# Kernel tuning notes

Measured on AMD Instinct MI355X. Metric: run time of the kernel, lower is better.

Reference implementation:

```python
import jax, jax.numpy as jnp
import numpy as np

B, D, H, STEPS = 32768, 8, 64, 100


def setup_inputs() -> dict:
    key = jax.random.key(0)
    ks = jax.random.split(key, 7)
    def lin(k, shape, fan_in):
        # torch nn.Linear default init: U(-1/sqrt(fan_in), 1/sqrt(fan_in))
        return jax.random.uniform(k, shape, jnp.float32, -1.0, 1.0) / np.sqrt(fan_in).astype(np.float32)
    return {
        "x0": jax.random.normal(ks[0], (B, D), jnp.float32),
        "W1": lin(ks[1], (H, D + 1), D + 1),
        "b1": lin(ks[2], (H,), D + 1),
        "W2": lin(ks[3], (H, H), H),
        "b2": lin(ks[4], (H,), H),
        "W3": lin(ks[5], (D, H), H),
        "b3": lin(ks[6], (D,), H),
        "num_steps": STEPS,
    }


def _mlp(x, t_col, W1, b1, W2, b2, W3, b3):
    # x: [B, D], t_col: [B, 1] -> dx/dt: [B, D]
    xt = jnp.concatenate([x, t_col], axis=1)          # [B, D+1]
    h = jnp.tanh(xt @ W1.T + b1)                      # [B, H]
    h = jnp.tanh(h @ W2.T + b2)                       # [B, H]
    return h @ W3.T + b3                              # [B, D]


def reference(x0, W1, b1, W2, b2, W3, b3, num_steps):
    t0, t1 = 0.0, 1.0
    dt = (t1 - t0) / num_steps
    n, d = x0.shape
    ones_out = jnp.ones((n, d), x0.dtype)

    def step(carry, i):
        x, ld = carry
        t_col = jnp.full((n, 1), t0, x0.dtype) + i.astype(x0.dtype) * dt
        dx = _mlp(x, t_col, W1, b1, W2, b2, W3, b3)
        x_new = x + dt * dx
        # Faithful to torch source: grad of dx_dt.sum() wrt x evaluated at the
        # POST-step x (this is J^T @ 1, then summed over input dims).
        f = lambda xx: _mlp(xx, t_col, W1, b1, W2, b2, W3, b3)
        _, vjp_fn = jax.vjp(f, x_new)
        (g,) = vjp_fn(ones_out)                       # [B, D]
        ld_new = ld + dt * g.sum(axis=1)
        return (x_new, ld_new), None

    init = (x0, jnp.zeros(n, x0.dtype))
    (x, log_det), _ = jax.lax.scan(step, init, jnp.arange(num_steps))
    return x, log_det
```

## Files before the change

### kernel.cpp

```cpp
#include <hip/hip_runtime.h>


__device__ float g_w1r[64];
__device__ float g_w3c[64];

__global__ void cnf_prep(const float* __restrict__ W1, const float* __restrict__ W3) {
    int h = threadIdx.x;
    float s = 0.f;
#pragma unroll
    for (int k = 0; k < 8; ++k) s += W1[h * 9 + k];
    g_w1r[h] = s;
    float c = 0.f;
#pragma unroll
    for (int d = 0; d < 8; ++d) c += W3[d * 64 + h];
    g_w3c[h] = c;
}

__device__ __forceinline__ float ftanh(float x) {
    float e = __builtin_amdgcn_exp2f(x * 2.885390081777926815f);
    float r = __builtin_amdgcn_rcpf(e + 1.0f);
    return fmaf(-2.0f, r, 1.0f);
}

typedef __attribute__((ext_vector_type(8))) short v8s;
typedef __attribute__((ext_vector_type(4))) float v4f;
typedef __attribute__((ext_vector_type(2))) float v2f;

union FragU {
    v8s s;
    unsigned u[4];
};

__device__ __forceinline__ unsigned pkbf(float a, float b) {
    unsigned ua = __builtin_bit_cast(unsigned, a) + 0x8000u;
    unsigned ub = __builtin_bit_cast(unsigned, b) + 0x8000u;
    return __builtin_amdgcn_perm(ub, ua, 0x07060302u);
}
__device__ __forceinline__ unsigned pkbf2(v2f v) { return pkbf(v.x, v.y); }

__device__ __forceinline__ int physj(int ks, int q, int jj) {
    return 16 * (ks + 2 * (jj >> 2)) + 4 * q + (jj & 3);
}

__device__ __forceinline__ void rename(const uint2 ph[4], FragU bh[2]) {
#pragma unroll
    for (int ks = 0; ks < 2; ++ks) {
        bh[ks].u[0] = ph[ks].x;
        bh[ks].u[1] = ph[ks].y;
        bh[ks].u[2] = ph[ks + 2].x;
        bh[ks].u[3] = ph[ks + 2].y;
    }
}

__global__ __launch_bounds__(256, 2) void cnf_fused(
    const float* __restrict__ x0, const float* __restrict__ W1,
    const float* __restrict__ b1, const float* __restrict__ W2,
    const float* __restrict__ b2, const float* __restrict__ W3,
    const float* __restrict__ b3, const int* __restrict__ nsp,
    float* __restrict__ out, int rows) {
    const int tid = threadIdx.x;
    const int w = tid >> 6;
    const int lane = tid & 63;
    const int c = lane & 15;
    const int q = lane >> 4;
    const int row0 = blockIdx.x * 64 + w * 16;

    const int n = *nsp;
    const float dt = 1.0f / (float)n;

    FragU a1[4];
#pragma unroll
    for (int mt = 0; mt < 4; ++mt) {
        const int m = 16 * mt + c;
        float f[8] = {0.f, 0.f, 0.f, 0.f, 0.f, 0.f, 0.f, 0.f};
        if (q == 0) {
#pragma unroll
            for (int jj = 0; jj < 4; ++jj) f[jj] = W1[m * 9 + jj];
            f[4] = W1[m * 9 + 8];
            f[5] = b1[m];
        } else if (q == 1) {
#pragma unroll
            for (int jj = 0; jj < 4; ++jj) f[jj] = W1[m * 9 + 4 + jj];
        }
#pragma unroll
        for (int p = 0; p < 4; ++p) a1[mt].u[p] = pkbf(f[2 * p], f[2 * p + 1]);
    }
    FragU a2[4][2], a2u[4][2], a2d[4][2];
#pragma unroll
    for (int mt = 0; mt < 4; ++mt)
#pragma unroll
        for (int ks = 0; ks < 2; ++ks) {
            const int m = 16 * mt + c;
            float f[8], fu[8], fd[8];
#pragma unroll
            for (int jj = 0; jj < 8; ++jj) {
                const int pj = physj(ks, q, jj);
                const float wv = W2[m * 64 + pj];
                f[jj] = wv;
                fu[jj] = wv * g_w1r[pj];
                fd[jj] = wv * (dt * W1[pj * 9 + 8]);
            }
#pragma unroll
            for (int p = 0; p < 4; ++p) {
                a2[mt][ks].u[p] = pkbf(f[2 * p], f[2 * p + 1]);
                a2u[mt][ks].u[p] = pkbf(fu[2 * p], fu[2 * p + 1]);
                a2d[mt][ks].u[p] = pkbf(fd[2 * p], fd[2 * p + 1]);
            }
        }
    FragU a3[2];
#pragma unroll
    for (int ks = 0; ks < 2; ++ks) {
        float f[8];
#pragma unroll
        for (int jj = 0; jj < 8; ++jj) f[jj] = W3[(c & 7) * 64 + physj(ks, q, jj)];
#pragma unroll
        for (int p = 0; p < 4; ++p) a3[ks].u[p] = pkbf(f[2 * p], f[2 * p + 1]);
    }
    v2f w3c01[4], w3c23[4];
    v4f vb2[4];
#pragma unroll
    for (int mt = 0; mt < 4; ++mt) {
        const int j0 = 16 * mt + 4 * q;
        vb2[mt][0] = b2[j0]; vb2[mt][1] = b2[j0 + 1];
        vb2[mt][2] = b2[j0 + 2]; vb2[mt][3] = b2[j0 + 3];
        w3c01[mt] = v2f{g_w3c[j0], g_w3c[j0 + 1]};
        w3c23[mt] = v2f{g_w3c[j0 + 2], g_w3c[j0 + 3]};
    }
    v4f vb3;
#pragma unroll
    for (int r = 0; r < 4; ++r) vb3[r] = b3[(4 * q + r) & 7];

    float xr[4];
    {
        float4 v = *(const float4*)(x0 + (size_t)(row0 + c) * 8 + 4 * (q & 1));
        xr[0] = v.x; xr[1] = v.y; xr[2] = v.z; xr[3] = v.w;
    }
    const v4f vzero = {0.f, 0.f, 0.f, 0.f};
    v2f gv = {0.f, 0.f};

    {
        FragU bx;
        bx.u[0] = pkbf(xr[0], xr[1]);
        bx.u[1] = pkbf(xr[2], xr[3]);
        bx.u[2] = pkbf(0.0f, 1.0f);
        bx.u[3] = 0u;
        v4f d1[4];
#pragma unroll
        for (int mt = 0; mt < 4; ++mt)
            d1[mt] = __builtin_amdgcn_mfma_f32_16x16x32_bf16(a1[mt].s, bx.s, vzero, 0, 0, 0);
        uint2 ph[4];
#pragma unroll
        for (int mt = 0; mt < 4; ++mt) {
            ph[mt].x = pkbf(ftanh(d1[mt][0]), ftanh(d1[mt][1]));
            ph[mt].y = pkbf(ftanh(d1[mt][2]), ftanh(d1[mt][3]));
        }
        FragU bh[2];
        rename(ph, bh);
        v4f d2[4];
#pragma unroll
        for (int mt = 0; mt < 4; ++mt) {
            d2[mt] = __builtin_amdgcn_mfma_f32_16x16x32_bf16(a2[mt][0].s, bh[0].s, vb2[mt], 0, 0, 0);
            d2[mt] = __builtin_amdgcn_mfma_f32_16x16x32_bf16(a2[mt][1].s, bh[1].s, d2[mt], 0, 0, 0);
        }
#pragma unroll
        for (int mt = 0; mt < 4; ++mt) {
            ph[mt].x = pkbf(ftanh(d2[mt][0]), ftanh(d2[mt][1]));
            ph[mt].y = pkbf(ftanh(d2[mt][2]), ftanh(d2[mt][3]));
        }
        FragU bh2[2];
        rename(ph, bh2);
        v4f d3;
        d3 = __builtin_amdgcn_mfma_f32_16x16x32_bf16(a3[0].s, bh2[0].s, vb3, 0, 0, 0);
        d3 = __builtin_amdgcn_mfma_f32_16x16x32_bf16(a3[1].s, bh2[1].s, d3, 0, 0, 0);
#pragma unroll
        for (int r = 0; r < 4; ++r) xr[r] = fmaf(dt, d3[r], xr[r]);
    }

    float tp = 0.0f;
    for (int i = 1; i < n; ++i) {
        FragU bx;
        bx.u[0] = pkbf(xr[0], xr[1]);
        bx.u[1] = pkbf(xr[2], xr[3]);
        bx.u[2] = pkbf(tp, 1.0f);
        bx.u[3] = 0u;
        tp += dt;
        v4f d1[4];
#pragma unroll
        for (int mt = 0; mt < 4; ++mt)
            d1[mt] = __builtin_amdgcn_mfma_f32_16x16x32_bf16(a1[mt].s, bx.s, vzero, 0, 0, 0);

        uint2 phb[4], pom[4];
#pragma unroll
        for (int mt = 0; mt < 4; ++mt) {
            v2f th01 = {ftanh(d1[mt][0]), ftanh(d1[mt][1])};
            v2f th23 = {ftanh(d1[mt][2]), ftanh(d1[mt][3])};
            v2f om01 = v2f{1.f, 1.f} - th01 * th01;
            v2f om23 = v2f{1.f, 1.f} - th23 * th23;
            phb[mt].x = pkbf2(th01);
            phb[mt].y = pkbf2(th23);
            pom[mt].x = pkbf2(om01);
            pom[mt].y = pkbf2(om23);
        }
        FragU bhb[2], bo[2];
        rename(phb, bhb);
        rename(pom, bo);

        v4f z2b[4], sv[4], dz2[4];
#pragma unroll
        for (int mt = 0; mt < 4; ++mt) {
            z2b[mt] = __builtin_amdgcn_mfma_f32_16x16x32_bf16(a2[mt][0].s, bhb[0].s, vb2[mt], 0, 0, 0);
            z2b[mt] = __builtin_amdgcn_mfma_f32_16x16x32_bf16(a2[mt][1].s, bhb[1].s, z2b[mt], 0, 0, 0);
            sv[mt] = __builtin_amdgcn_mfma_f32_16x16x32_bf16(a2u[mt][0].s, bo[0].s, vzero, 0, 0, 0);
            sv[mt] = __builtin_amdgcn_mfma_f32_16x16x32_bf16(a2u[mt][1].s, bo[1].s, sv[mt], 0, 0, 0);
            dz2[mt] = __builtin_amdgcn_mfma_f32_16x16x32_bf16(a2d[mt][0].s, bo[0].s, vzero, 0, 0, 0);
            dz2[mt] = __builtin_amdgcn_mfma_f32_16x16x32_bf16(a2d[mt][1].s, bo[1].s, dz2[mt], 0, 0, 0);
        }

        uint2 ph2[4];
#pragma unroll
        for (int mt = 0; mt < 4; ++mt) {
            v2f th01 = {ftanh(z2b[mt][0]), ftanh(z2b[mt][1])};
            v2f th23 = {ftanh(z2b[mt][2]), ftanh(z2b[mt][3])};
            v2f om01 = v2f{1.f, 1.f} - th01 * th01;
            v2f om23 = v2f{1.f, 1.f} - th23 * th23;
            gv += (w3c01[mt] * om01) * v2f{sv[mt][0], sv[mt][1]};
            gv += (w3c23[mt] * om23) * v2f{sv[mt][2], sv[mt][3]};
            v2f tf01 = om01 * v2f{dz2[mt][0], dz2[mt][1]} + th01;
            v2f tf23 = om23 * v2f{dz2[mt][2], dz2[mt][3]} + th23;
            ph2[mt].x = pkbf2(tf01);
            ph2[mt].y = pkbf2(tf23);
        }
        FragU bh2[2];
        rename(ph2, bh2);
        v4f d3;
        d3 = __builtin_amdgcn_mfma_f32_16x16x32_bf16(a3[0].s, bh2[0].s, vb3, 0, 0, 0);
        d3 = __builtin_amdgcn_mfma_f32_16x16x32_bf16(a3[1].s, bh2[1].s, d3, 0, 0, 0);
#pragma unroll
        for (int r = 0; r < 4; ++r) xr[r] = fmaf(dt, d3[r], xr[r]);
    }

    {
        FragU bx;
        bx.u[0] = pkbf(xr[0], xr[1]);
        bx.u[1] = pkbf(xr[2], xr[3]);
        bx.u[2] = pkbf(tp, 1.0f);
        bx.u[3] = 0u;
        v4f d1[4];
#pragma unroll
        for (int mt = 0; mt < 4; ++mt)
            d1[mt] = __builtin_amdgcn_mfma_f32_16x16x32_bf16(a1[mt].s, bx.s, vzero, 0, 0, 0);
        uint2 phb[4], pom[4];
#pragma unroll
        for (int mt = 0; mt < 4; ++mt) {
            v2f th01 = {ftanh(d1[mt][0]), ftanh(d1[mt][1])};
            v2f th23 = {ftanh(d1[mt][2]), ftanh(d1[mt][3])};
            v2f om01 = v2f{1.f, 1.f} - th01 * th01;
            v2f om23 = v2f{1.f, 1.f} - th23 * th23;
            phb[mt].x = pkbf2(th01);
            phb[mt].y = pkbf2(th23);
            pom[mt].x = pkbf2(om01);
            pom[mt].y = pkbf2(om23);
        }
        FragU bhb[2], bo[2];
        rename(phb, bhb);
        rename(pom, bo);
        v4f z2b[4], sv[4];
#pragma unroll
        for (int mt = 0; mt < 4; ++mt) {
            z2b[mt] = __builtin_amdgcn_mfma_f32_16x16x32_bf16(a2[mt][0].s, bhb[0].s, vb2[mt], 0, 0, 0);
            z2b[mt] = __builtin_amdgcn_mfma_f32_16x16x32_bf16(a2[mt][1].s, bhb[1].s, z2b[mt], 0, 0, 0);
            sv[mt] = __builtin_amdgcn_mfma_f32_16x16x32_bf16(a2u[mt][0].s, bo[0].s, vzero, 0, 0, 0);
            sv[mt] = __builtin_amdgcn_mfma_f32_16x16x32_bf16(a2u[mt][1].s, bo[1].s, sv[mt], 0, 0, 0);
        }
#pragma unroll
        for (int mt = 0; mt < 4; ++mt) {
            v2f th01 = {ftanh(z2b[mt][0]), ftanh(z2b[mt][1])};
            v2f th23 = {ftanh(z2b[mt][2]), ftanh(z2b[mt][3])};
            v2f om01 = v2f{1.f, 1.f} - th01 * th01;
            v2f om23 = v2f{1.f, 1.f} - th23 * th23;
            gv += (w3c01[mt] * om01) * v2f{sv[mt][0], sv[mt][1]};
            gv += (w3c23[mt] * om23) * v2f{sv[mt][2], sv[mt][3]};
        }
    }

    float g = gv.x + gv.y;
    g += __shfl_xor(g, 16);
    g += __shfl_xor(g, 32);
    if (q < 2) {
        float4 st = {xr[0], xr[1], xr[2], xr[3]};
        *(float4*)(out + (size_t)(row0 + c) * 8 + 4 * q) = st;
    }
    if (q == 0) out[(size_t)rows * 8 + row0 + c] = dt * g;
}

extern "C" void kernel_launch(void* const* d_in, const int* in_sizes, int n_in,
                              void* d_out, int out_size, void* d_ws, size_t ws_size,
                              hipStream_t stream) {
    const float* x0 = (const float*)d_in[0];
    const float* W1 = (const float*)d_in[1];
    const float* b1 = (const float*)d_in[2];
    const float* W2 = (const float*)d_in[3];
    const float* b2 = (const float*)d_in[4];
    const float* W3 = (const float*)d_in[5];
    const float* b3 = (const float*)d_in[6];
    const int* ns = (const int*)d_in[7];
    float* out = (float*)d_out;
    const int rows = in_sizes[0] / 8;

    hipLaunchKernelGGL(cnf_prep, dim3(1), dim3(64), 0, stream, W1, W3);
    hipLaunchKernelGGL(cnf_fused, dim3(rows / 64), dim3(256), 0, stream,
                       x0, W1, b1, W2, b2, W3, b3, ns, out, rows);
}
```

Measured before the change: 226.7 us.

## Switch MFMA operands to fp16 and fold tanh scale and w3c into weights

Replaces bf16 packing (add-and-perm) with the hardware cvt_pkrtz fp16 pack and swaps to f16 MFMA. Pre-multiplies W1, b1, W2 and b2 by the exp2 tanh scale so ftanh drops a multiply per element. Folds the w3c column sums into the a2u weight matrix so the gradient accumulation loses one multiply and eight registers. This trims VALU work in the step loop, at the cost of fp16 range and rounding risk from the scaled weights and round-toward-zero conversion.

```diff
diff --git a/kernel.cpp b/kernel.cpp
--- a/kernel.cpp
+++ b/kernel.cpp
@@ -1,5 +1,7 @@
 #include <hip/hip_runtime.h>
 
+
+#define TSCALE 2.885390081777926815f
 
 __device__ float g_w1r[64];
 __device__ float g_w3c[64];
@@ -16,27 +18,27 @@
     g_w3c[h] = c;
 }
 
-__device__ __forceinline__ float ftanh(float x) {
-    float e = __builtin_amdgcn_exp2f(x * 2.885390081777926815f);
+__device__ __forceinline__ float ftanh_s(float z) {
+    float e = __builtin_amdgcn_exp2f(z);
     float r = __builtin_amdgcn_rcpf(e + 1.0f);
     return fmaf(-2.0f, r, 1.0f);
 }
 
-typedef __attribute__((ext_vector_type(8))) short v8s;
+typedef __attribute__((ext_vector_type(8))) _Float16 v8h;
+typedef __attribute__((ext_vector_type(2))) __fp16 v2fp;
 typedef __attribute__((ext_vector_type(4))) float v4f;
 typedef __attribute__((ext_vector_type(2))) float v2f;
 
 union FragU {
-    v8s s;
+    v8h h;
     unsigned u[4];
 };
 
-__device__ __forceinline__ unsigned pkbf(float a, float b) {
-    unsigned ua = __builtin_bit_cast(unsigned, a) + 0x8000u;
-    unsigned ub = __builtin_bit_cast(unsigned, b) + 0x8000u;
-    return __builtin_amdgcn_perm(ub, ua, 0x07060302u);
-}
-__device__ __forceinline__ unsigned pkbf2(v2f v) { return pkbf(v.x, v.y); }
+__device__ __forceinline__ unsigned pk16(float a, float b) {
+    v2fp t = __builtin_amdgcn_cvt_pkrtz(a, b);
+    return __builtin_bit_cast(unsigned, t);
+}
+__device__ __forceinline__ unsigned pk16v(v2f v) { return pk16(v.x, v.y); }
 
 __device__ __forceinline__ int physj(int ks, int q, int jj) {
     return 16 * (ks + 2 * (jj >> 2)) + 4 * q + (jj & 3);
@@ -75,36 +77,37 @@
         float f[8] = {0.f, 0.f, 0.f, 0.f, 0.f, 0.f, 0.f, 0.f};
         if (q == 0) {
 #pragma unroll
-            for (int jj = 0; jj < 4; ++jj) f[jj] = W1[m * 9 + jj];
-            f[4] = W1[m * 9 + 8];
-            f[5] = b1[m];
+            for (int jj = 0; jj < 4; ++jj) f[jj] = TSCALE * W1[m * 9 + jj];
+            f[4] = TSCALE * W1[m * 9 + 8];
+            f[5] = TSCALE * b1[m];
         } else if (q == 1) {
 #pragma unroll
-            for (int jj = 0; jj < 4; ++jj) f[jj] = W1[m * 9 + 4 + jj];
-        }
-#pragma unroll
-        for (int p = 0; p < 4; ++p) a1[mt].u[p] = pkbf(f[2 * p], f[2 * p + 1]);
-    }
-    FragU a2[4][2], a2u[4][2], a2d[4][2];
+            for (int jj = 0; jj < 4; ++jj) f[jj] = TSCALE * W1[m * 9 + 4 + jj];
+        }
+#pragma unroll
+        for (int p = 0; p < 4; ++p) a1[mt].u[p] = pk16(f[2 * p], f[2 * p + 1]);
+    }
+    FragU a2[4][2], a2g[4][2], a2d[4][2];
 #pragma unroll
     for (int mt = 0; mt < 4; ++mt)
 #pragma unroll
         for (int ks = 0; ks < 2; ++ks) {
             const int m = 16 * mt + c;
-            float f[8], fu[8], fd[8];
+            const float w3cm = g_w3c[m];
+            float f[8], fg[8], fd[8];
 #pragma unroll
             for (int jj = 0; jj < 8; ++jj) {
                 const int pj = physj(ks, q, jj);
                 const float wv = W2[m * 64 + pj];
-                f[jj] = wv;
-                fu[jj] = wv * g_w1r[pj];
+                f[jj] = TSCALE * wv;
+                fg[jj] = w3cm * wv * g_w1r[pj];
                 fd[jj] = wv * (dt * W1[pj * 9 + 8]);
             }
 #pragma unroll
             for (int p = 0; p < 4; ++p) {
-                a2[mt][ks].u[p] = pkbf(f[2 * p], f[2 * p + 1]);
-                a2u[mt][ks].u[p] = pkbf(fu[2 * p], fu[2 * p + 1]);
-                a2d[mt][ks].u[p] = pkbf(fd[2 * p], fd[2 * p + 1]);
+                a2[mt][ks].u[p] = pk16(f[2 * p], f[2 * p + 1]);
+                a2g[mt][ks].u[p] = pk16(fg[2 * p], fg[2 * p + 1]);
+                a2d[mt][ks].u[p] = pk16(fd[2 * p], fd[2 * p + 1]);
             }
         }
     FragU a3[2];
@@ -114,17 +117,14 @@
 #pragma unroll
         for (int jj = 0; jj < 8; ++jj) f[jj] = W3[(c & 7) * 64 + physj(ks, q, jj)];
 #pragma unroll
-        for (int p = 0; p < 4; ++p) a3[ks].u[p] = pkbf(f[2 * p], f[2 * p + 1]);
-    }
-    v2f w3c01[4], w3c23[4];
+        for (int p = 0; p < 4; ++p) a3[ks].u[p] = pk16(f[2 * p], f[2 * p + 1]);
+    }
     v4f vb2[4];
 #pragma unroll
     for (int mt = 0; mt < 4; ++mt) {
         const int j0 = 16 * mt + 4 * q;
-        vb2[mt][0] = b2[j0]; vb2[mt][1] = b2[j0 + 1];
-        vb2[mt][2] = b2[j0 + 2]; vb2[mt][3] = b2[j0 + 3];
-        w3c01[mt] = v2f{g_w3c[j0], g_w3c[j0 + 1]};
-        w3c23[mt] = v2f{g_w3c[j0 + 2], g_w3c[j0 + 3]};
+        vb2[mt][0] = TSCALE * b2[j0]; vb2[mt][1] = TSCALE * b2[j0 + 1];
+        vb2[mt][2] = TSCALE * b2[j0 + 2]; vb2[mt][3] = TSCALE * b2[j0 + 3];
     }
     v4f vb3;
 #pragma unroll
@@ -140,38 +140,38 @@
 
     {
         FragU bx;
-        bx.u[0] = pkbf(xr[0], xr[1]);
-        bx.u[1] = pkbf(xr[2], xr[3]);
-        bx.u[2] = pkbf(0.0f, 1.0f);
+        bx.u[0] = pk16(xr[0], xr[1]);
+        bx.u[1] = pk16(xr[2], xr[3]);
+        bx.u[2] = pk16(0.0f, 1.0f);
         bx.u[3] = 0u;
         v4f d1[4];
 #pragma unroll
         for (int mt = 0; mt < 4; ++mt)
-            d1[mt] = __builtin_amdgcn_mfma_f32_16x16x32_bf16(a1[mt].s, bx.s, vzero, 0, 0, 0);
+            d1[mt] = __builtin_amdgcn_mfma_f32_16x16x32_f16(a1[mt].h, bx.h, vzero, 0, 0, 0);
         uint2 ph[4];
 #pragma unroll
         for (int mt = 0; mt < 4; ++mt) {
-            ph[mt].x = pkbf(ftanh(d1[mt][0]), ftanh(d1[mt][1]));
-            ph[mt].y = pkbf(ftanh(d1[mt][2]), ftanh(d1[mt][3]));
+            ph[mt].x = pk16(ftanh_s(d1[mt][0]), ftanh_s(d1[mt][1]));
+            ph[mt].y = pk16(ftanh_s(d1[mt][2]), ftanh_s(d1[mt][3]));
         }
         FragU bh[2];
         rename(ph, bh);
         v4f d2[4];
 #pragma unroll
         for (int mt = 0; mt < 4; ++mt) {
-            d2[mt] = __builtin_amdgcn_mfma_f32_16x16x32_bf16(a2[mt][0].s, bh[0].s, vb2[mt], 0, 0, 0);
-            d2[mt] = __builtin_amdgcn_mfma_f32_16x16x32_bf16(a2[mt][1].s, bh[1].s, d2[mt], 0, 0, 0);
-        }
-#pragma unroll
-        for (int mt = 0; mt < 4; ++mt) {
-            ph[mt].x = pkbf(ftanh(d2[mt][0]), ftanh(d2[mt][1]));
-            ph[mt].y = pkbf(ftanh(d2[mt][2]), ftanh(d2[mt][3]));
+            d2[mt] = __builtin_amdgcn_mfma_f32_16x16x32_f16(a2[mt][0].h, bh[0].h, vb2[mt], 0, 0, 0);
+            d2[mt] = __builtin_amdgcn_mfma_f32_16x16x32_f16(a2[mt][1].h, bh[1].h, d2[mt], 0, 0, 0);
+        }
+#pragma unroll
+        for (int mt = 0; mt < 4; ++mt) {
+            ph[mt].x = pk16(ftanh_s(d2[mt][0]), ftanh_s(d2[mt][1]));
+            ph[mt].y = pk16(ftanh_s(d2[mt][2]), ftanh_s(d2[mt][3]));
         }
         FragU bh2[2];
         rename(ph, bh2);
         v4f d3;
-        d3 = __builtin_amdgcn_mfma_f32_16x16x32_bf16(a3[0].s, bh2[0].s, vb3, 0, 0, 0);
-        d3 = __builtin_amdgcn_mfma_f32_16x16x32_bf16(a3[1].s, bh2[1].s, d3, 0, 0, 0);
+        d3 = __builtin_amdgcn_mfma_f32_16x16x32_f16(a3[0].h, bh2[0].h, vb3, 0, 0, 0);
+        d3 = __builtin_amdgcn_mfma_f32_16x16x32_f16(a3[1].h, bh2[1].h, d3, 0, 0, 0);
 #pragma unroll
         for (int r = 0; r < 4; ++r) xr[r] = fmaf(dt, d3[r], xr[r]);
     }
@@ -179,107 +179,107 @@
     float tp = 0.0f;
     for (int i = 1; i < n; ++i) {
         FragU bx;
-        bx.u[0] = pkbf(xr[0], xr[1]);
-        bx.u[1] = pkbf(xr[2], xr[3]);
-        bx.u[2] = pkbf(tp, 1.0f);
+        bx.u[0] = pk16(xr[0], xr[1]);
+        bx.u[1] = pk16(xr[2], xr[3]);
+        bx.u[2] = pk16(tp, 1.0f);
         bx.u[3] = 0u;
         tp += dt;
         v4f d1[4];
 #pragma unroll
         for (int mt = 0; mt < 4; ++mt)
-            d1[mt] = __builtin_amdgcn_mfma_f32_16x16x32_bf16(a1[mt].s, bx.s, vzero, 0, 0, 0);
+            d1[mt] = __builtin_amdgcn_mfma_f32_16x16x32_f16(a1[mt].h, bx.h, vzero, 0, 0, 0);
 
         uint2 phb[4], pom[4];
 #pragma unroll
         for (int mt = 0; mt < 4; ++mt) {
-            v2f th01 = {ftanh(d1[mt][0]), ftanh(d1[mt][1])};
-            v2f th23 = {ftanh(d1[mt][2]), ftanh(d1[mt][3])};
+            v2f th01 = {ftanh_s(d1[mt][0]), ftanh_s(d1[mt][1])};
+            v2f th23 = {ftanh_s(d1[mt][2]), ftanh_s(d1[mt][3])};
             v2f om01 = v2f{1.f, 1.f} - th01 * th01;
             v2f om23 = v2f{1.f, 1.f} - th23 * th23;
-            phb[mt].x = pkbf2(th01);
-            phb[mt].y = pkbf2(th23);
-            pom[mt].x = pkbf2(om01);
-            pom[mt].y = pkbf2(om23);
+            phb[mt].x = pk16v(th01);
+            phb[mt].y = pk16v(th23);
+            pom[mt].x = pk16v(om01);
+            pom[mt].y = pk16v(om23);
         }
         FragU bhb[2], bo[2];
         rename(phb, bhb);
         rename(pom, bo);
 
-        v4f z2b[4], sv[4], dz2[4];
-#pragma unroll
-        for (int mt = 0; mt < 4; ++mt) {
-            z2b[mt] = __builtin_amdgcn_mfma_f32_16x16x32_bf16(a2[mt][0].s, bhb[0].s, vb2[mt], 0, 0, 0);
-            z2b[mt] = __builtin_amdgcn_mfma_f32_16x16x32_bf16(a2[mt][1].s, bhb[1].s, z2b[mt], 0, 0, 0);
-            sv[mt] = __builtin_amdgcn_mfma_f32_16x16x32_bf16(a2u[mt][0].s, bo[0].s, vzero, 0, 0, 0);
-            sv[mt] = __builtin_amdgcn_mfma_f32_16x16x32_bf16(a2u[mt][1].s, bo[1].s, sv[mt], 0, 0, 0);
-            dz2[mt] = __builtin_amdgcn_mfma_f32_16x16x32_bf16(a2d[mt][0].s, bo[0].s, vzero, 0, 0, 0);
-            dz2[mt] = __builtin_amdgcn_mfma_f32_16x16x32_bf16(a2d[mt][1].s, bo[1].s, dz2[mt], 0, 0, 0);
+        v4f z2b[4], sg[4], dz2[4];
+#pragma unroll
+        for (int mt = 0; mt < 4; ++mt) {
+            z2b[mt] = __builtin_amdgcn_mfma_f32_16x16x32_f16(a2[mt][0].h, bhb[0].h, vb2[mt], 0, 0, 0);
+            z2b[mt] = __builtin_amdgcn_mfma_f32_16x16x32_f16(a2[mt][1].h, bhb[1].h, z2b[mt], 0, 0, 0);
+            sg[mt] = __builtin_amdgcn_mfma_f32_16x16x32_f16(a2g[mt][0].h, bo[0].h, vzero, 0, 0, 0);
+            sg[mt] = __builtin_amdgcn_mfma_f32_16x16x32_f16(a2g[mt][1].h, bo[1].h, sg[mt], 0, 0, 0);
+            dz2[mt] = __builtin_amdgcn_mfma_f32_16x16x32_f16(a2d[mt][0].h, bo[0].h, vzero, 0, 0, 0);
+            dz2[mt] = __builtin_amdgcn_mfma_f32_16x16x32_f16(a2d[mt][1].h, bo[1].h, dz2[mt], 0, 0, 0);
         }
 
         uint2 ph2[4];
 #pragma unroll
         for (int mt = 0; mt < 4; ++mt) {
-            v2f th01 = {ftanh(z2b[mt][0]), ftanh(z2b[mt][1])};
-            v2f th23 = {ftanh(z2b[mt][2]), ftanh(z2b[mt][3])};
+            v2f th01 = {ftanh_s(z2b[mt][0]), ftanh_s(z2b[mt][1])};
+            v2f th23 = {ftanh_s(z2b[mt][2]), ftanh_s(z2b[mt][3])};
             v2f om01 = v2f{1.f, 1.f} - th01 * th01;
             v2f om23 = v2f{1.f, 1.f} - th23 * th23;
-            gv += (w3c01[mt] * om01) * v2f{sv[mt][0], sv[mt][1]};
-            gv += (w3c23[mt] * om23) * v2f{sv[mt][2], sv[mt][3]};
+            gv += om01 * v2f{sg[mt][0], sg[mt][1]};
+            gv += om23 * v2f{sg[mt][2], sg[mt][3]};
             v2f tf01 = om01 * v2f{dz2[mt][0], dz2[mt][1]} + th01;
             v2f tf23 = om23 * v2f{dz2[mt][2], dz2[mt][3]} + th23;
-            ph2[mt].x = pkbf2(tf01);
-            ph2[mt].y = pkbf2(tf23);
+            ph2[mt].x = pk16v(tf01);
+            ph2[mt].y = pk16v(tf23);
         }
         FragU bh2[2];
         rename(ph2, bh2);
         v4f d3;
-        d3 = __builtin_amdgcn_mfma_f32_16x16x32_bf16(a3[0].s, bh2[0].s, vb3, 0, 0, 0);
-        d3 = __builtin_amdgcn_mfma_f32_16x16x32_bf16(a3[1].s, bh2[1].s, d3, 0, 0, 0);
+        d3 = __builtin_amdgcn_mfma_f32_16x16x32_f16(a3[0].h, bh2[0].h, vb3, 0, 0, 0);
+        d3 = __builtin_amdgcn_mfma_f32_16x16x32_f16(a3[1].h, bh2[1].h, d3, 0, 0, 0);
 #pragma unroll
         for (int r = 0; r < 4; ++r) xr[r] = fmaf(dt, d3[r], xr[r]);
     }
 
     {
         FragU bx;
-        bx.u[0] = pkbf(xr[0], xr[1]);
-        bx.u[1] = pkbf(xr[2], xr[3]);
-        bx.u[2] = pkbf(tp, 1.0f);
+        bx.u[0] = pk16(xr[0], xr[1]);
+        bx.u[1] = pk16(xr[2], xr[3]);
+        bx.u[2] = pk16(tp, 1.0f);
         bx.u[3] = 0u;
         v4f d1[4];
 #pragma unroll
         for (int mt = 0; mt < 4; ++mt)
-            d1[mt] = __builtin_amdgcn_mfma_f32_16x16x32_bf16(a1[mt].s, bx.s, vzero, 0, 0, 0);
+            d1[mt] = __builtin_amdgcn_mfma_f32_16x16x32_f16(a1[mt].h, bx.h, vzero, 0, 0, 0);
         uint2 phb[4], pom[4];
 #pragma unroll
         for (int mt = 0; mt < 4; ++mt) {
-            v2f th01 = {ftanh(d1[mt][0]), ftanh(d1[mt][1])};
-            v2f th23 = {ftanh(d1[mt][2]), ftanh(d1[mt][3])};
+            v2f th01 = {ftanh_s(d1[mt][0]), ftanh_s(d1[mt][1])};
+            v2f th23 = {ftanh_s(d1[mt][2]), ftanh_s(d1[mt][3])};
             v2f om01 = v2f{1.f, 1.f} - th01 * th01;
             v2f om23 = v2f{1.f, 1.f} - th23 * th23;
-            phb[mt].x = pkbf2(th01);
-            phb[mt].y = pkbf2(th23);
-            pom[mt].x = pkbf2(om01);
-            pom[mt].y = pkbf2(om23);
+            phb[mt].x = pk16v(th01);
+            phb[mt].y = pk16v(th23);
+            pom[mt].x = pk16v(om01);
+            pom[mt].y = pk16v(om23);
         }
         FragU bhb[2], bo[2];
         rename(phb, bhb);
         rename(pom, bo);
-        v4f z2b[4], sv[4];
-#pragma unroll
-        for (int mt = 0; mt < 4; ++mt) {
-            z2b[mt] = __builtin_amdgcn_mfma_f32_16x16x32_bf16(a2[mt][0].s, bhb[0].s, vb2[mt], 0, 0, 0);
-            z2b[mt] = __builtin_amdgcn_mfma_f32_16x16x32_bf16(a2[mt][1].s, bhb[1].s, z2b[mt], 0, 0, 0);
-            sv[mt] = __builtin_amdgcn_mfma_f32_16x16x32_bf16(a2u[mt][0].s, bo[0].s, vzero, 0, 0, 0);
-            sv[mt] = __builtin_amdgcn_mfma_f32_16x16x32_bf16(a2u[mt][1].s, bo[1].s, sv[mt], 0, 0, 0);
-        }
-#pragma unroll
-        for (int mt = 0; mt < 4; ++mt) {
-            v2f th01 = {ftanh(z2b[mt][0]), ftanh(z2b[mt][1])};
-            v2f th23 = {ftanh(z2b[mt][2]), ftanh(z2b[mt][3])};
+        v4f z2b[4], sg[4];
+#pragma unroll
+        for (int mt = 0; mt < 4; ++mt) {
+            z2b[mt] = __builtin_amdgcn_mfma_f32_16x16x32_f16(a2[mt][0].h, bhb[0].h, vb2[mt], 0, 0, 0);
+            z2b[mt] = __builtin_amdgcn_mfma_f32_16x16x32_f16(a2[mt][1].h, bhb[1].h, z2b[mt], 0, 0, 0);
+            sg[mt] = __builtin_amdgcn_mfma_f32_16x16x32_f16(a2g[mt][0].h, bo[0].h, vzero, 0, 0, 0);
+            sg[mt] = __builtin_amdgcn_mfma_f32_16x16x32_f16(a2g[mt][1].h, bo[1].h, sg[mt], 0, 0, 0);
+        }
+#pragma unroll
+        for (int mt = 0; mt < 4; ++mt) {
+            v2f th01 = {ftanh_s(z2b[mt][0]), ftanh_s(z2b[mt][1])};
+            v2f th23 = {ftanh_s(z2b[mt][2]), ftanh_s(z2b[mt][3])};
             v2f om01 = v2f{1.f, 1.f} - th01 * th01;
             v2f om23 = v2f{1.f, 1.f} - th23 * th23;
-            gv += (w3c01[mt] * om01) * v2f{sv[mt][0], sv[mt][1]};
-            gv += (w3c23[mt] * om23) * v2f{sv[mt][2], sv[mt][3]};
+            gv += om01 * v2f{sg[mt][0], sg[mt][1]};
+            gv += om23 * v2f{sg[mt][2], sg[mt][3]};
         }
     }
 
```

After: 204.6 us. -9.8%, faster.
